# Optimization experiments

Hardware: AMD Instinct MI355X
Metric: run time of the kernel (lower is better)

Reference implementation:

```python
import jax, jax.numpy as jnp
import numpy as np

NUM_NODES = 200000  # num_user + num_item
DIM_E = 64
NUM_EDGES = 600000
EPS = 1e-12
NEG_SLOPE = 0.01  # F.leaky_relu default


def setup_inputs() -> dict:
    key = jax.random.key(0)
    k1, k2, k3 = jax.random.split(key, 3)
    # xavier_normal on [N, D]: std = sqrt(2/(fan_in+fan_out))
    std = float(np.sqrt(2.0 / (NUM_NODES + DIM_E)))
    id_embedding = jax.random.normal(k1, (NUM_NODES, DIM_E), dtype=jnp.float32) * std
    edge_index = jax.random.randint(k2, (2, NUM_EDGES), 0, NUM_NODES, dtype=jnp.int64)
    weight_vector = jax.random.uniform(k3, (2 * NUM_EDGES, 1), dtype=jnp.float32)
    return {"id_embedding": id_embedding, "edge_index": edge_index,
            "weight_vector": weight_vector}


def _l2_normalize(x):
    # F.normalize(x, p=2, dim=1, eps=1e-12)
    n = jnp.sqrt(jnp.sum(x * x, axis=1, keepdims=True))
    return x / jnp.maximum(n, EPS)


def _leaky_relu(x):
    return jnp.where(x >= 0, x, NEG_SLOPE * x)


def reference(id_embedding, edge_index, weight_vector):
    N = id_embedding.shape[0]
    # symmetrize: cat(edge_index, edge_index[[1,0]])
    ei = jnp.concatenate([edge_index, edge_index[::-1]], axis=1)
    src, dst = ei[0], ei[1]  # messages flow src -> dst (PyG source_to_target)
    cnt = jax.ops.segment_sum(jnp.ones((src.shape[0],), jnp.float32), dst,
                              num_segments=N)[:, None]
    denom = jnp.maximum(cnt, 1.0)  # isolated nodes: sum is 0, mean defined as 0

    def conv(x):
        msg = x[src] * weight_vector            # gather + per-edge scale [2E, D]
        agg = jax.ops.segment_sum(msg, dst, num_segments=N)  # scatter-sum [N, D]
        return agg / denom                      # scatter-mean

    x = _l2_normalize(id_embedding)
    x1 = _leaky_relu(conv(x))
    x2 = _leaky_relu(conv(x1))
    return x + x1 + x2
```

## Files before the change

### kernel.cpp

```cpp
#include <hip/hip_runtime.h>
#include <hip/hip_fp16.h>

#define DIM 64
#define NEG_SLOPE 0.01f
#define BKT 256
#define TILEP 4096
#define RECS (TILEP * 2)
#define STILE 2048

typedef unsigned u32;
typedef unsigned short u16;
typedef unsigned char u8;


__global__ void k_norm_hist(const float* __restrict__ emb,
                            __half* __restrict__ x0h,
                            const int* __restrict__ p,
                            u32* __restrict__ mat,
                            int N, int E, int rb, int B, int nblkE) {
    int t = threadIdx.x;
    if ((int)blockIdx.x < rb) {
        int lane = t & 63;
        int row  = blockIdx.x * 32 + (t >> 6) * 4 + (lane >> 4);
        int l16  = lane & 15;
        if (row >= N) return;
        float4 v = *(const float4*)(emb + (size_t)row * DIM + l16 * 4);
        float s = v.x * v.x + v.y * v.y + v.z * v.z + v.w * v.w;
        #pragma unroll
        for (int m = 1; m < 16; m <<= 1) s += __shfl_xor(s, m, 64);
        float inv = 1.0f / fmaxf(sqrtf(s), 1e-12f);
        union { uint2 u; __half2 h[2]; } pk;
        pk.h[0] = __floats2half2_rn(v.x * inv, v.y * inv);
        pk.h[1] = __floats2half2_rn(v.z * inv, v.w * inv);
        *(uint2*)(x0h + (size_t)row * DIM + l16 * 4) = pk.u;
    } else {
        __shared__ u32 hist[800];
        int blk = blockIdx.x - rb;
        for (int i = t; i < B; i += 512) hist[i] = 0;
        __syncthreads();
        int base = blk * TILEP;
        #pragma unroll
        for (int k = 0; k < TILEP / 512; k++) {
            int pe = base + k * 512 + t;
            if (pe < E) {
                int a = p[pe];
                int b = p[pe + E];
                atomicAdd(&hist[(u32)b >> 8], 1u);
                atomicAdd(&hist[(u32)a >> 8], 1u);
            }
        }
        __syncthreads();
        for (int i = t; i < B; i += 512) mat[(size_t)i * nblkE + blk] = hist[i];
    }
}

__global__ void k_scan1(const u32* __restrict__ in, u32* __restrict__ out,
                        u32* __restrict__ bsum, int M) {
    __shared__ u32 sdata[256];
    int t = threadIdx.x;
    int base = blockIdx.x * STILE + t * 8;
    u32 v[8]; u32 tsum = 0;
    #pragma unroll
    for (int k = 0; k < 8; k++) {
        int i = base + k;
        v[k] = (i < M) ? in[i] : 0u;
        tsum += v[k];
    }
    sdata[t] = tsum;
    __syncthreads();
    for (int off = 1; off < 256; off <<= 1) {
        u32 x = (t >= off) ? sdata[t - off] : 0u;
        __syncthreads();
        sdata[t] += x;
        __syncthreads();
    }
    u32 run = sdata[t] - tsum;
    if (t == 255) bsum[blockIdx.x] = sdata[255];
    #pragma unroll
    for (int k = 0; k < 8; k++) {
        int i = base + k;
        if (i < M) out[i] = run;
        run += v[k];
    }
}

__global__ void k_scanfix(u32* __restrict__ mscan,
                          const u32* __restrict__ bsum, int nb, int M) {
    __shared__ u32 sdata[256];
    __shared__ u32 sexcl[256];
    int t = threadIdx.x;
    u32 v = (t < nb) ? bsum[t] : 0u;
    sdata[t] = v;
    __syncthreads();
    for (int off = 1; off < 256; off <<= 1) {
        u32 x = (t >= off) ? sdata[t - off] : 0u;
        __syncthreads();
        sdata[t] += x;
        __syncthreads();
    }
    sexcl[t] = sdata[t] - v;
    __syncthreads();
    int i = blockIdx.x * 256 + t;
    if (i < M) mscan[i] += sexcl[i >> 11];
}

__global__ __launch_bounds__(512, 1)
void k_place(const int* __restrict__ p, const float* __restrict__ w,
             const u32* __restrict__ mscan,
             u32* __restrict__ pay, u8* __restrict__ loc8,
             int E, int nblkE, int B) {
    __shared__ u32 sPay[RECS];
    __shared__ u32 sMeta[RECS];
    __shared__ u16 sPerm[RECS];
    __shared__ u32 hist[1024];
    __shared__ u32 sstart[1024];
    __shared__ u32 delta[1024];
    __shared__ u32 sdata[512];

    int blk = blockIdx.x;
    int t = threadIdx.x;
    int base = blk * TILEP;
    int rem = E - base;
    int vlim = rem * 2; if (vlim > RECS) vlim = RECS;

    hist[t] = 0; hist[t + 512] = 0;
    __syncthreads();

    #pragma unroll
    for (int k = 0; k < TILEP / 512; k++) {
        int pe = base + k * 512 + t;
        if (pe < E) {
            int a = p[pe];
            int b = p[pe + E];
            float wf = w[pe];
            float wb = w[pe + E];
            u32 wf14 = (u32)(wf * 16384.0f + 0.5f); if (wf14 > 16383u) wf14 = 16383u;
            u32 wb14 = (u32)(wb * 16384.0f + 0.5f); if (wb14 > 16383u) wb14 = 16383u;
            int li = (k * 512 + t) * 2;
            sPay[li]      = ((u32)a << 14) | wf14;
            sMeta[li]     = (u32)b;
            sPay[li + 1]  = ((u32)b << 14) | wb14;
            sMeta[li + 1] = (u32)a;
            atomicAdd(&hist[(u32)b >> 8], 1u);
            atomicAdd(&hist[(u32)a >> 8], 1u);
        }
    }
    __syncthreads();

    u32 a0 = hist[2 * t], a1 = hist[2 * t + 1];
    u32 tsum = a0 + a1;
    sdata[t] = tsum;
    __syncthreads();
    for (int off = 1; off < 512; off <<= 1) {
        u32 x = (t >= off) ? sdata[t - off] : 0u;
        __syncthreads();
        sdata[t] += x;
        __syncthreads();
    }
    u32 texcl = sdata[t] - tsum;
    sstart[2 * t]     = texcl;
    sstart[2 * t + 1] = texcl + a0;
    __syncthreads();

    hist[t] = 0; hist[t + 512] = 0;
    for (int i = t; i < B; i += 512)
        delta[i] = mscan[(size_t)i * nblkE + blk] - sstart[i];
    __syncthreads();

    #pragma unroll
    for (int k = 0; k < RECS / 512; k++) {
        int li = k * 512 + t;
        if (li < vlim) {
            u32 bin = sMeta[li] >> 8;
            u32 r = atomicAdd(&hist[bin], 1u);
            sPerm[sstart[bin] + r] = (u16)li;
        }
    }
    __syncthreads();

    #pragma unroll
    for (int k = 0; k < RECS / 512; k++) {
        int j = k * 512 + t;
        if (j < vlim) {
            int li = sPerm[j];
            u32 pv = sPay[li];
            u32 mt = sMeta[li];
            u32 gs = (u32)j + delta[mt >> 8];
            pay[gs]  = pv;
            loc8[gs] = (u8)(mt & 255u);
        }
    }
}

__global__ void k_bucket(const u32* __restrict__ pay,
                         const u8* __restrict__ loc8,
                         const u32* __restrict__ mscan,
                         u32* __restrict__ row_ptr,
                         u32* __restrict__ colw,
                         int N, int E, int B, int nblkE) {
    __shared__ u32 hist[BKT];
    __shared__ u32 excl[BKT];
    __shared__ u32 sdata[256];
    int b = blockIdx.x;
    int t = threadIdx.x;
    int node0 = b * BKT;
    int nnodes = N - node0; if (nnodes > BKT) nnodes = BKT;
    size_t flat0 = (size_t)b * nblkE;
    u32 seg_s = mscan[flat0];
    u32 seg_e = (b + 1 < B) ? mscan[flat0 + nblkE] : (u32)(2 * E);
    hist[t] = 0;
    __syncthreads();
    for (u32 j = seg_s + t; j < seg_e; j += 256)
        atomicAdd(&hist[loc8[j]], 1u);
    __syncthreads();
    u32 tsum = hist[t];
    sdata[t] = tsum;
    __syncthreads();
    for (int off = 1; off < 256; off <<= 1) {
        u32 x = (t >= off) ? sdata[t - off] : 0u;
        __syncthreads();
        sdata[t] += x;
        __syncthreads();
    }
    u32 texcl = sdata[t] - tsum;
    excl[t] = texcl;
    if (t < nnodes) row_ptr[node0 + t] = seg_s + texcl;
    if (b == 0 && t == 0) row_ptr[N] = (u32)(2 * E);
    __syncthreads();
    for (u32 j = seg_s + t; j < seg_e; j += 256) {
        u32 loc = loc8[j];
        u32 pos = atomicAdd(&excl[loc], 1u);
        colw[seg_s + pos] = pay[j];
    }
}


__device__ __forceinline__ void gather8(const __half* __restrict__ x,
                                        const u32* __restrict__ colw,
                                        u32 s, u32 e, int g, int sub,
                                        float acc[8]) {
    for (u32 base = s; base < e; base += 8) {
        int m = (int)(e - base); if (m > 8) m = 8;
        u32 u = 0;
        if (sub < m) u = colw[base + sub];
        int   cx = (int)(u >> 14);
        float cy = (float)(u & 16383u) * (1.0f / 16384.0f);
        for (int j = 0; j < m; j++) {
            int   sj = __shfl(cx, (g << 3) | j, 64);
            float wj = __shfl(cy, (g << 3) | j, 64);
            uint4 q = *(const uint4*)(x + (size_t)sj * DIM + sub * 8);
            const __half2* hp = (const __half2*)&q;
            #pragma unroll
            for (int k = 0; k < 4; k++) {
                float2 f = __half22float2(hp[k]);
                acc[2 * k]     += f.x * wj;
                acc[2 * k + 1] += f.y * wj;
            }
        }
    }
}

__global__ void k_conv1(const __half* __restrict__ x0h,
                        const u32* __restrict__ row_ptr,
                        const u32* __restrict__ colw,
                        __half* __restrict__ x1h, int N) {
    int wave = (blockIdx.x * 256 + threadIdx.x) >> 6;
    int g    = (threadIdx.x >> 3) & 7;
    int sub  = threadIdx.x & 7;
    int row  = wave * 8 + g;
    if (row >= N) return;
    u32 s = row_ptr[row], e = row_ptr[row + 1];
    float acc[8] = {0, 0, 0, 0, 0, 0, 0, 0};
    gather8(x0h, colw, s, e, g, sub, acc);
    float rdeno = 1.0f / fmaxf((float)(e - s), 1.0f);
    __half2 hv[4];
    #pragma unroll
    for (int k = 0; k < 4; k++) {
        float v0 = acc[2 * k] * rdeno;
        float v1 = acc[2 * k + 1] * rdeno;
        v0 = (v0 >= 0.0f) ? v0 : NEG_SLOPE * v0;
        v1 = (v1 >= 0.0f) ? v1 : NEG_SLOPE * v1;
        hv[k] = __floats2half2_rn(v0, v1);
    }
    *(uint4*)(x1h + (size_t)row * DIM + sub * 8) = *(const uint4*)hv;
}

__global__ void k_conv2(const __half* __restrict__ x0h,
                        const __half* __restrict__ x1h,
                        const u32* __restrict__ row_ptr,
                        const u32* __restrict__ colw,
                        float* __restrict__ out, int N) {
    int wave = (blockIdx.x * 256 + threadIdx.x) >> 6;
    int g    = (threadIdx.x >> 3) & 7;
    int sub  = threadIdx.x & 7;
    int row  = wave * 8 + g;
    if (row >= N) return;
    u32 s = row_ptr[row], e = row_ptr[row + 1];
    float acc[8] = {0, 0, 0, 0, 0, 0, 0, 0};
    gather8(x1h, colw, s, e, g, sub, acc);
    float rdeno = 1.0f / fmaxf((float)(e - s), 1.0f);
    uint4 q0 = *(const uint4*)(x0h + (size_t)row * DIM + sub * 8);
    uint4 q1 = *(const uint4*)(x1h + (size_t)row * DIM + sub * 8);
    const __half2* h0 = (const __half2*)&q0;
    const __half2* h1 = (const __half2*)&q1;
    float r[8];
    #pragma unroll
    for (int k = 0; k < 4; k++) {
        float2 a = __half22float2(h0[k]);
        float2 b = __half22float2(h1[k]);
        float x2a = acc[2 * k] * rdeno;
        float x2b = acc[2 * k + 1] * rdeno;
        x2a = (x2a >= 0.0f) ? x2a : NEG_SLOPE * x2a;
        x2b = (x2b >= 0.0f) ? x2b : NEG_SLOPE * x2b;
        r[2 * k]     = a.x + b.x + x2a;
        r[2 * k + 1] = a.y + b.y + x2b;
    }
    float* op = out + (size_t)row * DIM + sub * 8;
    *(float4*)(op)     = make_float4(r[0], r[1], r[2], r[3]);
    *(float4*)(op + 4) = make_float4(r[4], r[5], r[6], r[7]);
}

static inline size_t align16(size_t x) { return (x + 15) & ~(size_t)15; }

extern "C" void kernel_launch(void* const* d_in, const int* in_sizes, int n_in,
                              void* d_out, int out_size, void* d_ws, size_t ws_size,
                              hipStream_t stream) {
    const int N = in_sizes[0] / DIM;
    const int E = in_sizes[1] / 2;

    const float* emb = (const float*)d_in[0];
    const int*   ei  = (const int*)d_in[1];
    const float* w   = (const float*)d_in[2];
    float*       out = (float*)d_out;

    const int B     = (N + BKT - 1) / BKT;
    const int nblkE = (E + TILEP - 1) / TILEP;
    const int M     = B * nblkE;
    const int nb1   = (M + STILE - 1) / STILE;
    const int rb    = (N + 31) / 32;
    const int cvb   = (N + 31) / 32;

    char* ws = (char*)d_ws;
    size_t off = 0;
    __half* x0h    = (__half*)(ws + off); off += align16((size_t)N * DIM * 2);
    __half* x1h    = (__half*)(ws + off); off += align16((size_t)N * DIM * 2);
    u32*    pay    = (u32*)(ws + off);    off += align16((size_t)2 * E * 4);
    u8*     loc8   = (u8*)(ws + off);     off += align16((size_t)2 * E);
    u32*    colw   = (u32*)(ws + off);    off += align16((size_t)2 * E * 4);
    u32*    mat    = (u32*)(ws + off);    off += align16((size_t)M * 4);
    u32*    mscan  = (u32*)(ws + off);    off += align16((size_t)M * 4);
    u32*    row_ptr= (u32*)(ws + off);    off += align16((size_t)(N + 1) * 4);
    u32*    bsum   = (u32*)(ws + off);    off += align16(256 * 4);

    k_norm_hist<<<rb + nblkE, 512, 0, stream>>>(emb, x0h, ei, mat, N, E, rb, B, nblkE);
    k_scan1  <<<nb1, 256, 0, stream>>>(mat, mscan, bsum, M);
    k_scanfix<<<(M + 255) / 256, 256, 0, stream>>>(mscan, bsum, nb1, M);
    k_place  <<<nblkE, 512, 0, stream>>>(ei, w, mscan, pay, loc8, E, nblkE, B);
    k_bucket <<<B, 256, 0, stream>>>(pay, loc8, mscan, row_ptr, colw, N, E, B, nblkE);

    k_conv1<<<cvb, 256, 0, stream>>>(x0h, row_ptr, colw, x1h, N);
    k_conv2<<<cvb, 256, 0, stream>>>(x0h, x1h, row_ptr, colw, out, N);
}
```

Measured before the change: 210.7 us.

## Replace per-block histogram matrix scan with global atomic bucket counters

Drops the two-pass scan over the bucket-by-block count matrix. Each edge block now atomically adds its local histogram into a global per-bucket histogram, and each placement block redundantly scans that small histogram and claims its slots with atomics on a global cursor. This removes two kernel launches and the large matrix traffic, at the cost of a memset and atomic contention. Within a bucket, records are no longer ordered by block, so placement becomes nondeterministic. It also hoists the self-row loads in conv2 ahead of the gather.

```diff
diff --git a/kernel.cpp b/kernel.cpp
--- a/kernel.cpp
+++ b/kernel.cpp
@@ -6,7 +6,6 @@
 #define BKT 256
 #define TILEP 4096
 #define RECS (TILEP * 2)
-#define STILE 2048
 
 typedef unsigned u32;
 typedef unsigned short u16;
@@ -16,8 +15,8 @@
 __global__ void k_norm_hist(const float* __restrict__ emb,
                             __half* __restrict__ x0h,
                             const int* __restrict__ p,
-                            u32* __restrict__ mat,
-                            int N, int E, int rb, int B, int nblkE) {
+                            u32* __restrict__ ghist,
+                            int N, int E, int rb, int B) {
     int t = threadIdx.x;
     if ((int)blockIdx.x < rb) {
         int lane = t & 63;
@@ -50,65 +49,17 @@
             }
         }
         __syncthreads();
-        for (int i = t; i < B; i += 512) mat[(size_t)i * nblkE + blk] = hist[i];
-    }
-}
-
-__global__ void k_scan1(const u32* __restrict__ in, u32* __restrict__ out,
-                        u32* __restrict__ bsum, int M) {
-    __shared__ u32 sdata[256];
-    int t = threadIdx.x;
-    int base = blockIdx.x * STILE + t * 8;
-    u32 v[8]; u32 tsum = 0;
-    #pragma unroll
-    for (int k = 0; k < 8; k++) {
-        int i = base + k;
-        v[k] = (i < M) ? in[i] : 0u;
-        tsum += v[k];
-    }
-    sdata[t] = tsum;
-    __syncthreads();
-    for (int off = 1; off < 256; off <<= 1) {
-        u32 x = (t >= off) ? sdata[t - off] : 0u;
-        __syncthreads();
-        sdata[t] += x;
-        __syncthreads();
-    }
-    u32 run = sdata[t] - tsum;
-    if (t == 255) bsum[blockIdx.x] = sdata[255];
-    #pragma unroll
-    for (int k = 0; k < 8; k++) {
-        int i = base + k;
-        if (i < M) out[i] = run;
-        run += v[k];
-    }
-}
-
-__global__ void k_scanfix(u32* __restrict__ mscan,
-                          const u32* __restrict__ bsum, int nb, int M) {
-    __shared__ u32 sdata[256];
-    __shared__ u32 sexcl[256];
-    int t = threadIdx.x;
-    u32 v = (t < nb) ? bsum[t] : 0u;
-    sdata[t] = v;
-    __syncthreads();
-    for (int off = 1; off < 256; off <<= 1) {
-        u32 x = (t >= off) ? sdata[t - off] : 0u;
-        __syncthreads();
-        sdata[t] += x;
-        __syncthreads();
-    }
-    sexcl[t] = sdata[t] - v;
-    __syncthreads();
-    int i = blockIdx.x * 256 + t;
-    if (i < M) mscan[i] += sexcl[i >> 11];
+        for (int i = t; i < B; i += 512)
+            if (hist[i]) atomicAdd(&ghist[i], hist[i]);
+    }
 }
 
 __global__ __launch_bounds__(512, 1)
 void k_place(const int* __restrict__ p, const float* __restrict__ w,
-             const u32* __restrict__ mscan,
+             const u32* __restrict__ ghist, u32* __restrict__ gcur,
+             u32* __restrict__ gbase,
              u32* __restrict__ pay, u8* __restrict__ loc8,
-             int E, int nblkE, int B) {
+             int E, int B) {
     __shared__ u32 sPay[RECS];
     __shared__ u32 sMeta[RECS];
     __shared__ u16 sPerm[RECS];
@@ -122,6 +73,26 @@
     int base = blk * TILEP;
     int rem = E - base;
     int vlim = rem * 2; if (vlim > RECS) vlim = RECS;
+
+    u32 g0 = (2 * t     < B) ? ghist[2 * t]     : 0u;
+    u32 g1 = (2 * t + 1 < B) ? ghist[2 * t + 1] : 0u;
+    u32 gts = g0 + g1;
+    sdata[t] = gts;
+    __syncthreads();
+    for (int off = 1; off < 512; off <<= 1) {
+        u32 x = (t >= off) ? sdata[t - off] : 0u;
+        __syncthreads();
+        sdata[t] += x;
+        __syncthreads();
+    }
+    u32 gexcl = sdata[t] - gts;
+    delta[2 * t]     = gexcl;
+    delta[2 * t + 1] = gexcl + g0;
+    __syncthreads();
+    if (blk == 0) {
+        for (int i = t; i < B; i += 512) gbase[i] = delta[i];
+        if (t == 0) gbase[B] = (u32)(2 * E);
+    }
 
     hist[t] = 0; hist[t + 512] = 0;
     __syncthreads();
@@ -162,9 +133,15 @@
     sstart[2 * t + 1] = texcl + a0;
     __syncthreads();
 
+    for (int i = t; i < B; i += 512) {
+        u32 cnt = hist[i];
+        if (cnt) {
+            u32 off0 = atomicAdd(&gcur[i], cnt);
+            delta[i] = delta[i] + off0 - sstart[i];
+        }
+    }
+    __syncthreads();
     hist[t] = 0; hist[t + 512] = 0;
-    for (int i = t; i < B; i += 512)
-        delta[i] = mscan[(size_t)i * nblkE + blk] - sstart[i];
     __syncthreads();
 
     #pragma unroll
@@ -194,10 +171,10 @@
 
 __global__ void k_bucket(const u32* __restrict__ pay,
                          const u8* __restrict__ loc8,
-                         const u32* __restrict__ mscan,
+                         const u32* __restrict__ gbase,
                          u32* __restrict__ row_ptr,
                          u32* __restrict__ colw,
-                         int N, int E, int B, int nblkE) {
+                         int N, int E, int B) {
     __shared__ u32 hist[BKT];
     __shared__ u32 excl[BKT];
     __shared__ u32 sdata[256];
@@ -205,9 +182,8 @@
     int t = threadIdx.x;
     int node0 = b * BKT;
     int nnodes = N - node0; if (nnodes > BKT) nnodes = BKT;
-    size_t flat0 = (size_t)b * nblkE;
-    u32 seg_s = mscan[flat0];
-    u32 seg_e = (b + 1 < B) ? mscan[flat0 + nblkE] : (u32)(2 * E);
+    u32 seg_s = gbase[b];
+    u32 seg_e = gbase[b + 1];
     hist[t] = 0;
     __syncthreads();
     for (u32 j = seg_s + t; j < seg_e; j += 256)
@@ -296,11 +272,11 @@
     int row  = wave * 8 + g;
     if (row >= N) return;
     u32 s = row_ptr[row], e = row_ptr[row + 1];
+    uint4 q0 = *(const uint4*)(x0h + (size_t)row * DIM + sub * 8);
+    uint4 q1 = *(const uint4*)(x1h + (size_t)row * DIM + sub * 8);
     float acc[8] = {0, 0, 0, 0, 0, 0, 0, 0};
     gather8(x1h, colw, s, e, g, sub, acc);
     float rdeno = 1.0f / fmaxf((float)(e - s), 1.0f);
-    uint4 q0 = *(const uint4*)(x0h + (size_t)row * DIM + sub * 8);
-    uint4 q1 = *(const uint4*)(x1h + (size_t)row * DIM + sub * 8);
     const __half2* h0 = (const __half2*)&q0;
     const __half2* h1 = (const __half2*)&q1;
     float r[8];
@@ -335,8 +311,6 @@
 
     const int B     = (N + BKT - 1) / BKT;
     const int nblkE = (E + TILEP - 1) / TILEP;
-    const int M     = B * nblkE;
-    const int nb1   = (M + STILE - 1) / STILE;
     const int rb    = (N + 31) / 32;
     const int cvb   = (N + 31) / 32;
 
@@ -347,16 +321,17 @@
     u32*    pay    = (u32*)(ws + off);    off += align16((size_t)2 * E * 4);
     u8*     loc8   = (u8*)(ws + off);     off += align16((size_t)2 * E);
     u32*    colw   = (u32*)(ws + off);    off += align16((size_t)2 * E * 4);
-    u32*    mat    = (u32*)(ws + off);    off += align16((size_t)M * 4);
-    u32*    mscan  = (u32*)(ws + off);    off += align16((size_t)M * 4);
+    u32*    gmeta  = (u32*)(ws + off);    off += align16(1600 * 4);
+    u32*    gbase  = (u32*)(ws + off);    off += align16(800 * 4);
     u32*    row_ptr= (u32*)(ws + off);    off += align16((size_t)(N + 1) * 4);
-    u32*    bsum   = (u32*)(ws + off);    off += align16(256 * 4);
-
-    k_norm_hist<<<rb + nblkE, 512, 0, stream>>>(emb, x0h, ei, mat, N, E, rb, B, nblkE);
-    k_scan1  <<<nb1, 256, 0, stream>>>(mat, mscan, bsum, M);
-    k_scanfix<<<(M + 255) / 256, 256, 0, stream>>>(mscan, bsum, nb1, M);
-    k_place  <<<nblkE, 512, 0, stream>>>(ei, w, mscan, pay, loc8, E, nblkE, B);
-    k_bucket <<<B, 256, 0, stream>>>(pay, loc8, mscan, row_ptr, colw, N, E, B, nblkE);
+
+    u32* ghist = gmeta;
+    u32* gcur  = gmeta + 800;
+
+    hipMemsetAsync(gmeta, 0, 1600 * 4, stream);
+    k_norm_hist<<<rb + nblkE, 512, 0, stream>>>(emb, x0h, ei, ghist, N, E, rb, B);
+    k_place <<<nblkE, 512, 0, stream>>>(ei, w, ghist, gcur, gbase, pay, loc8, E, B);
+    k_bucket<<<B, 256, 0, stream>>>(pay, loc8, gbase, row_ptr, colw, N, E, B);
 
     k_conv1<<<cvb, 256, 0, stream>>>(x0h, row_ptr, colw, x1h, N);
     k_conv2<<<cvb, 256, 0, stream>>>(x0h, x1h, row_ptr, colw, out, N);
```

New measurement: 205.4 us. -2.5%, faster.
